# Kernel optimization log

Hardware: AMD Instinct MI355X
Metric: run time of the kernel (lower is better)

Reference implementation:

```python
import jax, jax.numpy as jnp
import numpy as np

TAU = 1.0
L = -0.1
R = 1.1
COUPLING_K = 2.0
EPS = 1e-6
LN_EPS = 1e-5


def entmax15(x, axis=-1):
    # Peters & Martins alpha=1.5 entmax via sort + threshold search.
    x = x / 2.0
    x = x - jnp.max(x, axis=axis, keepdims=True)
    xs = jnp.flip(jnp.sort(x, axis=axis), axis=axis)  # descending
    k = x.shape[axis]
    rho = jnp.arange(1, k + 1, dtype=x.dtype)
    mean = jnp.cumsum(xs, axis=axis) / rho
    mean_sq = jnp.cumsum(xs * xs, axis=axis) / rho
    ss = rho * (mean_sq - mean * mean)
    delta = jnp.clip((1.0 - ss) / rho, 0.0, None)
    tau = mean - jnp.sqrt(delta)
    support_size = jnp.sum(tau <= xs, axis=axis, keepdims=True)
    tau_star = jnp.take_along_axis(tau, support_size - 1, axis=axis)
    y = jnp.clip(x - tau_star, 0.0, None)
    return y * y


def setup_inputs() -> dict:
    key = jax.random.key(0)
    ks = jax.random.split(key, 4)
    B, S, D, H = 32, 4096, 768, 1024
    return {
        "embeddings": jax.random.normal(ks[0], (B, S, D), dtype=jnp.float32),
        "attn": jnp.ones((B, S), dtype=jnp.float32),
        "u": jax.random.uniform(ks[1], (B, S), dtype=jnp.float32),
        "ln_g": jnp.ones((D,), dtype=jnp.float32),
        "ln_b": jnp.zeros((D,), dtype=jnp.float32),
        "w1": jax.random.normal(ks[2], (H, D), dtype=jnp.float32) * 0.02,
        "b1": jnp.zeros((H,), dtype=jnp.float32),
        "w2": jax.random.normal(ks[3], (1, H), dtype=jnp.float32) * 0.02,
        "b2": jnp.zeros((1,), dtype=jnp.float32),
    }


def reference(embeddings, attn, u, ln_g, ln_b, w1, b1, w2, b2):
    # mask embeddings
    emb = embeddings * attn[..., None]                       # [B,S,D]
    # LayerNorm
    mu = jnp.mean(emb, axis=-1, keepdims=True)
    var = jnp.mean((emb - mu) ** 2, axis=-1, keepdims=True)
    x = (emb - mu) / jnp.sqrt(var + LN_EPS) * ln_g + ln_b
    # MLP scorer (dropout = identity in eval)
    h1 = jax.nn.gelu(jnp.einsum("bsd,hd->bsh", x, w1) + b1, approximate=False)
    scores = (jnp.einsum("bsh,oh->bso", h1, w2) + b2)[..., 0]  # [B,S]
    scores = jnp.where(attn == 0, -1e9, scores)
    # sparse attention over sequence axis
    z = entmax15(scores / TAU, axis=1) * attn
    # Kumaraswamy relaxed sampling with coupling
    eff = scores + COUPLING_K * (2.0 * z - 1.0)
    a = jax.nn.softplus(eff) + EPS
    b = jax.nn.softplus(-eff) + EPS
    uc = jnp.clip(u, EPS, 1.0 - EPS)
    xk = (1.0 - (1.0 - uc) ** (1.0 / b)) ** (1.0 / a)
    y = L + (R - L) * xk
    h = (jnp.clip(y, 0.0, 1.0) > 0.5).astype(scores.dtype) * attn
    # straight-through gate
    g = jax.lax.stop_gradient(h - z) + z
    reg = jnp.zeros((), dtype=scores.dtype)
    return (z, g, reg)
```

## Files before the change

### kernel.cpp

```cpp
#include <hip/hip_runtime.h>
#include <math.h>

#define NB 32
#define NS 4096
#define ND 768
#define NH 1024
#define NTOK (NB*NS)
#define NKC (ND/32)

typedef __bf16 bf16_t;
typedef __bf16 bf16x8 __attribute__((ext_vector_type(8)));
typedef float  f32x4  __attribute__((ext_vector_type(4)));

__global__ __launch_bounds__(256) void k_lnstats(
    const float* __restrict__ emb, const float* __restrict__ attn,
    float* __restrict__ mu_o, float* __restrict__ rs_o)
{
    const int token = blockIdx.x * 4 + (threadIdx.x >> 6);
    const int lane  = threadIdx.x & 63;
    const float am  = attn[token];
    const float* row = emb + (size_t)token * ND;

    float e[12];
    {
        const float4 v0 = *(const float4*)(row + lane * 4);
        const float4 v1 = *(const float4*)(row + 256 + lane * 4);
        const float4 v2 = *(const float4*)(row + 512 + lane * 4);
        e[0]=v0.x; e[1]=v0.y; e[2]=v0.z; e[3]=v0.w;
        e[4]=v1.x; e[5]=v1.y; e[6]=v1.z; e[7]=v1.w;
        e[8]=v2.x; e[9]=v2.y; e[10]=v2.z; e[11]=v2.w;
    }
    float s = 0.f;
#pragma unroll
    for (int j = 0; j < 12; j++) { e[j] *= am; s += e[j]; }
#pragma unroll
    for (int m = 32; m; m >>= 1) s += __shfl_xor(s, m, 64);
    const float mu = s * (1.0f / ND);

    float v = 0.f;
#pragma unroll
    for (int j = 0; j < 12; j++) { float d = e[j] - mu; v += d * d; }
#pragma unroll
    for (int m = 32; m; m >>= 1) v += __shfl_xor(v, m, 64);
    v *= (1.0f / ND);

    if (lane == 0) {
        mu_o[token] = mu;
        rs_o[token] = (float)(1.0 / sqrt((double)v + 1e-5));
    }
}

__global__ __launch_bounds__(256) void k_wprep(
    const float* __restrict__ w1, bf16_t* __restrict__ whB, bf16_t* __restrict__ wlB)
{
    const int t   = blockIdx.x * 256 + threadIdx.x;
    const int ln  = t & 63;
    const int h16 = (t >> 6) & 63;
    const int c   = t >> 12;
    const int row = h16 * 16 + (ln >> 2);
    const int k0  = c * 32 + 8 * ((ln & 3) ^ (ln >> 4));

    const float4 a = *(const float4*)(w1 + (size_t)row * ND + k0);
    const float4 b = *(const float4*)(w1 + (size_t)row * ND + k0 + 4);
    const float vv[8] = {a.x,a.y,a.z,a.w,b.x,b.y,b.z,b.w};
    bf16x8 hi, lo;
#pragma unroll
    for (int j = 0; j < 8; j++) {
        const bf16_t hj = (bf16_t)vv[j];
        hi[j] = hj;
        lo[j] = (bf16_t)(vv[j] - (float)hj);
    }
    const size_t o = (size_t)t * 8;
    *(bf16x8*)(whB + o) = hi;
    *(bf16x8*)(wlB + o) = lo;
}

#define TM 64
#define KC 32

__global__ __launch_bounds__(256, 2) void k_scorer(
    const float* __restrict__ emb, const float* __restrict__ attn,
    const float* __restrict__ ln_g, const float* __restrict__ ln_b,
    const bf16_t* __restrict__ whB, const bf16_t* __restrict__ wlB,
    const float* __restrict__ b1, const float* __restrict__ w2,
    const float* __restrict__ b2v,
    const float* __restrict__ mu_a, const float* __restrict__ rs_a,
    float* __restrict__ scores)
{
    __shared__ __align__(16) bf16_t sWh[256*32];
    __shared__ __align__(16) bf16_t sWl[256*32];
    __shared__ __align__(16) bf16_t sXh[64*32];
    __shared__ __align__(16) bf16_t sXl[64*32];
    __shared__ float sred[4*64];

    const int tid    = threadIdx.x;
    const int lane   = tid & 63;
    const int wv     = tid >> 6;
    const int token0 = blockIdx.x * TM;

    const int xt  = tid >> 2;
    const int xp  = tid & 3;
    const int xk8 = 8 * (xp ^ ((xt >> 2) & 3));
    const float x_mu = mu_a[token0 + xt];
    const float x_rs = rs_a[token0 + xt];
    const float x_at = attn[token0 + xt];
    const float* embrow = emb + (size_t)(token0 + xt) * ND;

    const int cn  = lane & 15;
    const int cq  = lane >> 4;
    const int fsw = (cq ^ (cn >> 2)) << 3;

    f32x4 acc[4][4];
    float spart[16];
#pragma unroll
    for (int i = 0; i < 16; i++) spart[i] = 0.f;

    for (int hq = 0; hq < 4; hq++) {
#pragma unroll
        for (int tt = 0; tt < 4; tt++)
#pragma unroll
            for (int ht = 0; ht < 4; ht++) acc[tt][ht] = (f32x4){0.f, 0.f, 0.f, 0.f};

        for (int kc = 0; kc < ND; kc += KC) {
            __syncthreads();
            {
                const size_t blk = ((size_t)((kc >> 5) * 64 + hq * 16 + wv * 4)) * 512 + lane * 8;
                const bf16_t* gh = whB + blk;
                const bf16_t* gl = wlB + blk;
#pragma unroll
                for (int i = 0; i < 4; i++)
                    __builtin_amdgcn_global_load_lds(
                        (const __attribute__((address_space(1))) void*)(gh + i * 512),
                        (__attribute__((address_space(3))) void*)&sWh[(wv*64 + i*16)*32],
                        16, 0, 0);
#pragma unroll
                for (int i = 0; i < 4; i++)
                    __builtin_amdgcn_global_load_lds(
                        (const __attribute__((address_space(1))) void*)(gl + i * 512),
                        (__attribute__((address_space(3))) void*)&sWl[(wv*64 + i*16)*32],
                        16, 0, 0);
            }
            {
                const float4 e0 = *(const float4*)(embrow + kc + xk8);
                const float4 e1 = *(const float4*)(embrow + kc + xk8 + 4);
                const float4 g0 = *(const float4*)(ln_g + kc + xk8);
                const float4 g1 = *(const float4*)(ln_g + kc + xk8 + 4);
                const float4 c0 = *(const float4*)(ln_b + kc + xk8);
                const float4 c1 = *(const float4*)(ln_b + kc + xk8 + 4);
                const float ev[8] = {e0.x,e0.y,e0.z,e0.w,e1.x,e1.y,e1.z,e1.w};
                const float gv[8] = {g0.x,g0.y,g0.z,g0.w,g1.x,g1.y,g1.z,g1.w};
                const float cv[8] = {c0.x,c0.y,c0.z,c0.w,c1.x,c1.y,c1.z,c1.w};
                bf16x8 hi, lo;
#pragma unroll
                for (int j = 0; j < 8; j++) {
                    const float x = (ev[j] * x_at - x_mu) * x_rs * gv[j] + cv[j];
                    const bf16_t hb = (bf16_t)x;
                    hi[j] = hb;
                    lo[j] = (bf16_t)(x - (float)hb);
                }
                *(bf16x8*)&sXh[xt*32 + xp*8] = hi;
                *(bf16x8*)&sXl[xt*32 + xp*8] = lo;
            }
            __syncthreads();
            bf16x8 ah[4], al[4];
#pragma unroll
            for (int tt = 0; tt < 4; tt++) {
                const int off = (tt*16 + cn)*32 + fsw;
                ah[tt] = *(const bf16x8*)&sXh[off];
                al[tt] = *(const bf16x8*)&sXl[off];
            }
#pragma unroll
            for (int ht = 0; ht < 4; ht++) {
                const int off = (wv*64 + ht*16 + cn)*32 + fsw;
                const bf16x8 bh = *(const bf16x8*)&sWh[off];
                const bf16x8 bl = *(const bf16x8*)&sWl[off];
#pragma unroll
                for (int tt = 0; tt < 4; tt++) {
                    acc[tt][ht] = __builtin_amdgcn_mfma_f32_16x16x32_bf16(ah[tt], bh, acc[tt][ht], 0, 0, 0);
                    acc[tt][ht] = __builtin_amdgcn_mfma_f32_16x16x32_bf16(al[tt], bh, acc[tt][ht], 0, 0, 0);
                    acc[tt][ht] = __builtin_amdgcn_mfma_f32_16x16x32_bf16(ah[tt], bl, acc[tt][ht], 0, 0, 0);
                }
            }
        }
#pragma unroll
        for (int ht = 0; ht < 4; ht++) {
            const int hg = hq*256 + wv*64 + ht*16 + cn;
            const float b1v = b1[hg];
            const float w2v = w2[hg];
#pragma unroll
            for (int tt = 0; tt < 4; tt++)
#pragma unroll
                for (int r = 0; r < 4; r++) {
                    const float pre = acc[tt][ht][r] + b1v;
                    const float ge  = 0.5f * pre * (1.0f + erff(pre * 0.70710678118654752f));
                    spart[tt*4 + r] += ge * w2v;
                }
        }
    }
#pragma unroll
    for (int i = 0; i < 16; i++) {
        float s = spart[i];
        s += __shfl_xor(s, 1, 64);
        s += __shfl_xor(s, 2, 64);
        s += __shfl_xor(s, 4, 64);
        s += __shfl_xor(s, 8, 64);
        spart[i] = s;
    }
    if (cn == 0) {
#pragma unroll
        for (int tt = 0; tt < 4; tt++)
#pragma unroll
            for (int r = 0; r < 4; r++)
                sred[wv*64 + tt*16 + cq*4 + r] = spart[tt*4 + r];
    }
    __syncthreads();
    if (tid < TM) {
        scores[token0 + tid] = sred[tid] + sred[64 + tid] + sred[128 + tid] + sred[192 + tid] + b2v[0];
    }
}

static __device__ __forceinline__ double softplus_d(double x) {
    return (x > 30.0) ? x : log1p(exp(x));
}

__global__ __launch_bounds__(1024) void k_taugate(
    const float* __restrict__ scores, const float* __restrict__ attn,
    const float* __restrict__ u, float* __restrict__ out)
{
    const int b    = blockIdx.x;
    const int tid  = threadIdx.x;
    const int lane = tid & 63;
    const int wid  = tid >> 6;

    __shared__ double redd[2][16];
    __shared__ float  redf[16];
    __shared__ float  bcf;

    float vv[4], at[4], sm[4];
#pragma unroll
    for (int j = 0; j < 4; j++) {
        const int i = tid + 1024 * j;
        at[j] = attn[b * NS + i];
        const float s = scores[b * NS + i];
        sm[j] = (at[j] == 0.0f) ? -1e9f : s;
        vv[j] = sm[j] * 0.5f;
    }

    float mx = fmaxf(fmaxf(vv[0], vv[1]), fmaxf(vv[2], vv[3]));
#pragma unroll
    for (int m = 32; m; m >>= 1) mx = fmaxf(mx, __shfl_xor(mx, m, 64));
    if (lane == 0) redf[wid] = mx;
    __syncthreads();
    if (tid == 0) {
        float t = redf[0];
        for (int i = 1; i < 16; i++) t = fmaxf(t, redf[i]);
        bcf = t;
    }
    __syncthreads();
    const double mxd = (double)bcf;

    double d[4];
#pragma unroll
    for (int j = 0; j < 4; j++) d[j] = (double)vv[j] - mxd;

    double lo = -1.0, hi = 0.0;
    for (int it = 0; it < 44; it++) {
        const double mid = 0.5 * (lo + hi);
        double s = 0.0;
#pragma unroll
        for (int j = 0; j < 4; j++) {
            const double t = d[j] - mid;
            if (t > 0.0) s += t * t;
        }
#pragma unroll
        for (int m = 32; m; m >>= 1) s += __shfl_xor(s, m, 64);
        const int p = it & 1;
        if (lane == 0) redd[p][wid] = s;
        __syncthreads();
        double tot = 0.0;
#pragma unroll
        for (int i = 0; i < 16; i++) tot += redd[p][i];
        if (tot >= 1.0) lo = mid; else hi = mid;
    }
    const double tau = lo;

    if (b == 0 && tid == 0) out[2 * NTOK] = 0.0f;

#pragma unroll
    for (int j = 0; j < 4; j++) {
        const int i = tid + 1024 * j;
        const double t  = d[j] - tau;
        const double zz = (t > 0.0) ? t * t : 0.0;
        const float  z  = (float)zz * at[j];

        const double eff  = (double)sm[j] + 2.0 * (2.0 * (double)z - 1.0);
        const double sp_p = softplus_d(eff)  + 1e-6;
        const double sp_n = softplus_d(-eff) + 1e-6;
        const double uc   = fmin(fmax((double)u[b * NS + i], 1e-6), 1.0 - 1e-6);
        const double xk   = pow(1.0 - pow(1.0 - uc, 1.0 / sp_n), 1.0 / sp_p);
        const double y    = -0.1 + 1.2 * xk;
        const double ycl  = fmin(fmax(y, 0.0), 1.0);
        float h = (ycl > 0.5) ? 1.0f : 0.0f;
        h *= at[j];
        const float g = (h - z) + z;

        out[b * NS + i]        = z;
        out[NTOK + b * NS + i] = g;
    }
}

extern "C" void kernel_launch(void* const* d_in, const int* in_sizes, int n_in,
                              void* d_out, int out_size, void* d_ws, size_t ws_size,
                              hipStream_t stream)
{
    const float* emb  = (const float*)d_in[0];
    const float* attn = (const float*)d_in[1];
    const float* u    = (const float*)d_in[2];
    const float* ln_g = (const float*)d_in[3];
    const float* ln_b = (const float*)d_in[4];
    const float* w1   = (const float*)d_in[5];
    const float* b1   = (const float*)d_in[6];
    const float* w2   = (const float*)d_in[7];
    const float* b2   = (const float*)d_in[8];
    float* out = (float*)d_out;

    float*  wsf    = (float*)d_ws;
    float*  scores = wsf;
    float*  mu     = wsf + NTOK;
    float*  rs     = wsf + 2 * NTOK;
    bf16_t* w1hB   = (bf16_t*)(wsf + 3 * NTOK);
    bf16_t* w1lB   = w1hB + (size_t)NH * ND;

    hipLaunchKernelGGL(k_lnstats, dim3(NTOK / 4), dim3(256), 0, stream,
                       emb, attn, mu, rs);
    hipLaunchKernelGGL(k_wprep, dim3((NKC * 64 * 64) / 256), dim3(256), 0, stream,
                       w1, w1hB, w1lB);
    hipLaunchKernelGGL(k_scorer, dim3(NTOK / TM), dim3(256), 0, stream,
                       emb, attn, ln_g, ln_b, w1hB, w1lB, b1, w2, b2, mu, rs, scores);
    hipLaunchKernelGGL(k_taugate, dim3(NB), dim3(1024), 0, stream,
                       scores, attn, u, out);
}
```

Baseline: 1.359 ms.

## Double-buffer weight tiles and prefetch activations in scorer GEMM loop

Gives the scorer kernel two LDS buffers for the weight tiles. The next weight chunk is issued via global_load_lds and the next embedding/LN parameters are loaded into registers before the MFMAs on the current chunk run, so global latency overlaps compute. It adds 32 KB of LDS per block, which may limit the two-blocks-per-CU occupancy target. It also raises register pressure from the prefetched float4s, and each iteration still has two barriers.

```diff
diff --git a/kernel.cpp b/kernel.cpp
--- a/kernel.cpp
+++ b/kernel.cpp
@@ -87,8 +87,8 @@
     const float* __restrict__ mu_a, const float* __restrict__ rs_a,
     float* __restrict__ scores)
 {
-    __shared__ __align__(16) bf16_t sWh[256*32];
-    __shared__ __align__(16) bf16_t sWl[256*32];
+    __shared__ __align__(16) bf16_t sWh[2][256*32];
+    __shared__ __align__(16) bf16_t sWl[2][256*32];
     __shared__ __align__(16) bf16_t sXh[64*32];
     __shared__ __align__(16) bf16_t sXl[64*32];
     __shared__ float sred[4*64];
@@ -115,53 +115,70 @@
 #pragma unroll
     for (int i = 0; i < 16; i++) spart[i] = 0.f;
 
+    float4 xe0, xe1, xg0, xg1, xb0, xb1;
+
+    auto loadX = [&](int c) {
+        const int kc = c * KC;
+        xe0 = *(const float4*)(embrow + kc + xk8);
+        xe1 = *(const float4*)(embrow + kc + xk8 + 4);
+        xg0 = *(const float4*)(ln_g + kc + xk8);
+        xg1 = *(const float4*)(ln_g + kc + xk8 + 4);
+        xb0 = *(const float4*)(ln_b + kc + xk8);
+        xb1 = *(const float4*)(ln_b + kc + xk8 + 4);
+    };
+    auto storeX = [&]() {
+        const float ev[8] = {xe0.x,xe0.y,xe0.z,xe0.w,xe1.x,xe1.y,xe1.z,xe1.w};
+        const float gv[8] = {xg0.x,xg0.y,xg0.z,xg0.w,xg1.x,xg1.y,xg1.z,xg1.w};
+        const float cv[8] = {xb0.x,xb0.y,xb0.z,xb0.w,xb1.x,xb1.y,xb1.z,xb1.w};
+        bf16x8 hi, lo;
+#pragma unroll
+        for (int j = 0; j < 8; j++) {
+            const float x = (ev[j] * x_at - x_mu) * x_rs * gv[j] + cv[j];
+            const bf16_t hb = (bf16_t)x;
+            hi[j] = hb;
+            lo[j] = (bf16_t)(x - (float)hb);
+        }
+        *(bf16x8*)&sXh[xt*32 + xp*8] = hi;
+        *(bf16x8*)&sXl[xt*32 + xp*8] = lo;
+    };
+    auto issueW = [&](int hq, int c, int buf) {
+        const size_t blk = ((size_t)(c * 64 + hq * 16 + wv * 4)) * 512 + lane * 8;
+        const bf16_t* gh = whB + blk;
+        const bf16_t* gl = wlB + blk;
+#pragma unroll
+        for (int i = 0; i < 4; i++)
+            __builtin_amdgcn_global_load_lds(
+                (const __attribute__((address_space(1))) void*)(gh + i * 512),
+                (__attribute__((address_space(3))) void*)&sWh[buf][(wv*64 + i*16)*32],
+                16, 0, 0);
+#pragma unroll
+        for (int i = 0; i < 4; i++)
+            __builtin_amdgcn_global_load_lds(
+                (const __attribute__((address_space(1))) void*)(gl + i * 512),
+                (__attribute__((address_space(3))) void*)&sWl[buf][(wv*64 + i*16)*32],
+                16, 0, 0);
+    };
+
+    loadX(0);
+    issueW(0, 0, 0);
+    storeX();
+    __syncthreads();
+
+    int cur = 0;
     for (int hq = 0; hq < 4; hq++) {
 #pragma unroll
         for (int tt = 0; tt < 4; tt++)
 #pragma unroll
             for (int ht = 0; ht < 4; ht++) acc[tt][ht] = (f32x4){0.f, 0.f, 0.f, 0.f};
 
-        for (int kc = 0; kc < ND; kc += KC) {
-            __syncthreads();
-            {
-                const size_t blk = ((size_t)((kc >> 5) * 64 + hq * 16 + wv * 4)) * 512 + lane * 8;
-                const bf16_t* gh = whB + blk;
-                const bf16_t* gl = wlB + blk;
-#pragma unroll
-                for (int i = 0; i < 4; i++)
-                    __builtin_amdgcn_global_load_lds(
-                        (const __attribute__((address_space(1))) void*)(gh + i * 512),
-                        (__attribute__((address_space(3))) void*)&sWh[(wv*64 + i*16)*32],
-                        16, 0, 0);
-#pragma unroll
-                for (int i = 0; i < 4; i++)
-                    __builtin_amdgcn_global_load_lds(
-                        (const __attribute__((address_space(1))) void*)(gl + i * 512),
-                        (__attribute__((address_space(3))) void*)&sWl[(wv*64 + i*16)*32],
-                        16, 0, 0);
+        for (int c = 0; c < 24; c++) {
+            const bool lastiter = (hq == 3) && (c == 23);
+            if (!lastiter) {
+                const int nhq = (c == 23) ? hq + 1 : hq;
+                const int nc  = (c == 23) ? 0 : c + 1;
+                loadX(nc);
+                issueW(nhq, nc, cur ^ 1);
             }
-            {
-                const float4 e0 = *(const float4*)(embrow + kc + xk8);
-                const float4 e1 = *(const float4*)(embrow + kc + xk8 + 4);
-                const float4 g0 = *(const float4*)(ln_g + kc + xk8);
-                const float4 g1 = *(const float4*)(ln_g + kc + xk8 + 4);
-                const float4 c0 = *(const float4*)(ln_b + kc + xk8);
-                const float4 c1 = *(const float4*)(ln_b + kc + xk8 + 4);
-                const float ev[8] = {e0.x,e0.y,e0.z,e0.w,e1.x,e1.y,e1.z,e1.w};
-                const float gv[8] = {g0.x,g0.y,g0.z,g0.w,g1.x,g1.y,g1.z,g1.w};
-                const float cv[8] = {c0.x,c0.y,c0.z,c0.w,c1.x,c1.y,c1.z,c1.w};
-                bf16x8 hi, lo;
-#pragma unroll
-                for (int j = 0; j < 8; j++) {
-                    const float x = (ev[j] * x_at - x_mu) * x_rs * gv[j] + cv[j];
-                    const bf16_t hb = (bf16_t)x;
-                    hi[j] = hb;
-                    lo[j] = (bf16_t)(x - (float)hb);
-                }
-                *(bf16x8*)&sXh[xt*32 + xp*8] = hi;
-                *(bf16x8*)&sXl[xt*32 + xp*8] = lo;
-            }
-            __syncthreads();
             bf16x8 ah[4], al[4];
 #pragma unroll
             for (int tt = 0; tt < 4; tt++) {
@@ -172,8 +189,8 @@
 #pragma unroll
             for (int ht = 0; ht < 4; ht++) {
                 const int off = (wv*64 + ht*16 + cn)*32 + fsw;
-                const bf16x8 bh = *(const bf16x8*)&sWh[off];
-                const bf16x8 bl = *(const bf16x8*)&sWl[off];
+                const bf16x8 bh = *(const bf16x8*)&sWh[cur][off];
+                const bf16x8 bl = *(const bf16x8*)&sWl[cur][off];
 #pragma unroll
                 for (int tt = 0; tt < 4; tt++) {
                     acc[tt][ht] = __builtin_amdgcn_mfma_f32_16x16x32_bf16(ah[tt], bh, acc[tt][ht], 0, 0, 0);
@@ -181,6 +198,10 @@
                     acc[tt][ht] = __builtin_amdgcn_mfma_f32_16x16x32_bf16(ah[tt], bl, acc[tt][ht], 0, 0, 0);
                 }
             }
+            __syncthreads();
+            if (!lastiter) storeX();
+            __syncthreads();
+            cur ^= 1;
         }
 #pragma unroll
         for (int ht = 0; ht < 4; ht++) {
```

Measured after the change: 1.365 ms. No clear change (+0.4%).
